# Kernel tuning notes

Measured on AMD Instinct MI355X. Metric: run time of the kernel, lower is better.

Reference implementation:

```python
import jax, jax.numpy as jnp
import numpy as np

EPS = float(np.finfo(np.float32).eps)


def setup_inputs() -> dict:
    key = jax.random.key(0)
    k1, k2, k3, k4 = jax.random.split(key, 4)
    B, M, N = 16, 200000, 200000
    xyzs1 = jax.random.normal(k1, (B, M, 3), dtype=jnp.float32)
    xyzs2 = jax.random.normal(k2, (B, M, 3), dtype=jnp.float32)
    pred_pairs = jax.random.randint(k3, (B, N, 2), 0, M)
    weights = jax.random.uniform(k4, (B, 1, N), dtype=jnp.float32)
    return {"xyzs1": xyzs1, "xyzs2": xyzs2, "pred_pairs": pred_pairs, "weights": weights}


def _weighted_procrustes(X, Y, w):
    # X, Y: [B, N, 3]; w: [B, N, 1]. DGR-style weighted Kabsch/Procrustes.
    W1 = jnp.abs(w).sum(axis=1, keepdims=True)            # [B, 1, 1]
    w_norm = w / (W1 + EPS)                               # [B, N, 1]
    mux = (w_norm * X).sum(axis=1, keepdims=True)         # [B, 1, 3]
    muy = (w_norm * Y).sum(axis=1, keepdims=True)         # [B, 1, 3]
    # Sxy = (Y - muy)^T @ (w_norm * (X - mux)) per sample -> [B, 3, 3]
    Sxy = jnp.einsum('bni,bnj->bij', Y - muy, w_norm * (X - mux))
    U, _, Vh = jnp.linalg.svd(Sxy)                        # Sxy = U diag(s) Vh
    # reflection fix: diag(1, 1, sign(det(U) * det(V)))
    d = jnp.where(jnp.linalg.det(U) * jnp.linalg.det(Vh) < 0, -1.0, 1.0)  # [B]
    S = jnp.concatenate([jnp.ones((X.shape[0], 2), dtype=U.dtype), d[:, None]], axis=1)
    R = (U * S[:, None, :]) @ Vh                          # U @ diag(S) @ V^T
    t = muy[:, 0, :] - jnp.einsum('bij,bj->bi', R, mux[:, 0, :])  # [B, 3]
    return R, t


def reference(xyzs1, xyzs2, pred_pairs, weights):
    w = jnp.transpose(weights, (0, 2, 1))                 # [B, N, 1]
    # batched gather of correspondences
    X = jax.vmap(lambda pts, idx: pts[idx])(xyzs1, pred_pairs[:, :, 0])
    Y = jax.vmap(lambda pts, idx: pts[idx])(xyzs2, pred_pairs[:, :, 1])
    Rs, ts = _weighted_procrustes(X, Y, w)
    ws = w.sum(axis=(1, 2))                               # per-sample weight sums
    return Rs, ts, ws
```

## Files before the change

### kernel.cpp

```cpp
#include <hip/hip_runtime.h>
#include <math.h>

#define BPB 96
#define NACC 17

typedef float  floatx4 __attribute__((ext_vector_type(4)));
typedef unsigned long long ullx2 __attribute__((ext_vector_type(2)));

struct __attribute__((packed, aligned(4))) f4 { float x, y, z, w; };

__device__ __forceinline__ void gather_pt(const float* __restrict__ base, int idx,
                                          bool guard, int M1,
                                          float& p0, float& p1, float& p2)
{
    const size_t o = 3 * (size_t)idx;
    if (guard && __builtin_expect(idx == M1, 0)) {
        p0 = base[o]; p1 = base[o + 1]; p2 = base[o + 2];
    } else {
        const f4 v = *(const f4*)(base + o);
        p0 = v.x; p1 = v.y; p2 = v.z;
    }
}

template <bool GUARD>
__device__ __forceinline__ void wp_loop(
    const float* __restrict__ x1b, const float* __restrict__ x2b,
    const ullx2* __restrict__ pv, const floatx4* __restrict__ wv,
    int c0, int stride, int nChunks, int M1, float acc[NACC])
{
    for (int c = c0; c < nChunks; c += stride) {
        const ullx2  pA = __builtin_nontemporal_load(&pv[2 * c]);
        const ullx2  pB = __builtin_nontemporal_load(&pv[2 * c + 1]);
        const floatx4 w4 = __builtin_nontemporal_load(&wv[c]);

        int ix[4], iy[4];
        ix[0] = (int)(unsigned)(pA.x & 0xffffffffu); iy[0] = (int)(unsigned)(pA.x >> 32);
        ix[1] = (int)(unsigned)(pA.y & 0xffffffffu); iy[1] = (int)(unsigned)(pA.y >> 32);
        ix[2] = (int)(unsigned)(pB.x & 0xffffffffu); iy[2] = (int)(unsigned)(pB.x >> 32);
        ix[3] = (int)(unsigned)(pB.y & 0xffffffffu); iy[3] = (int)(unsigned)(pB.y >> 32);

        float X[4][3], Y[4][3];
#pragma unroll
        for (int u = 0; u < 4; ++u)
            gather_pt(x1b, ix[u], GUARD, M1, X[u][0], X[u][1], X[u][2]);
#pragma unroll
        for (int u = 0; u < 4; ++u)
            gather_pt(x2b, iy[u], GUARD, M1, Y[u][0], Y[u][1], Y[u][2]);

#pragma unroll
        for (int u = 0; u < 4; ++u) {
            const float w = w4[u];
            acc[0] += fabsf(w);
            acc[1] += w;
            acc[2] += w * X[u][0];
            acc[3] += w * X[u][1];
            acc[4] += w * X[u][2];
            const float wy0 = w * Y[u][0], wy1 = w * Y[u][1], wy2 = w * Y[u][2];
            acc[5] += wy0; acc[6] += wy1; acc[7] += wy2;
            acc[8]  += wy0 * X[u][0]; acc[9]  += wy0 * X[u][1]; acc[10] += wy0 * X[u][2];
            acc[11] += wy1 * X[u][0]; acc[12] += wy1 * X[u][1]; acc[13] += wy1 * X[u][2];
            acc[14] += wy2 * X[u][0]; acc[15] += wy2 * X[u][1]; acc[16] += wy2 * X[u][2];
        }
    }
}

__global__ __launch_bounds__(256) void wp_partials(
    const float* __restrict__ xyzs1,
    const float* __restrict__ xyzs2,
    const int*   __restrict__ pairs,
    const float* __restrict__ weights,
    float* __restrict__ partials,
    int B, int M, int N)
{
    int b, ib;
    if ((B & 7) == 0) {
        const int grp = blockIdx.x / (8 * BPB);
        const int r   = blockIdx.x % (8 * BPB);
        b  = grp * 8 + (r & 7);
        ib = r >> 3;
    } else {
        b  = blockIdx.x % B;
        ib = blockIdx.x / B;
    }
    const int tid = threadIdx.x;

    const float* __restrict__ x1b = xyzs1 + (size_t)b * M * 3;
    const float* __restrict__ x2b = xyzs2 + (size_t)b * M * 3;
    const ullx2* __restrict__ pv  = (const ullx2*)(pairs + (size_t)b * N * 2);
    const floatx4* __restrict__ wv = (const floatx4*)(weights + (size_t)b * N);

    const bool lastBatch = (b == B - 1);
    const int  M1 = M - 1;
    const int  nChunks = N >> 2;

    float acc[NACC];
#pragma unroll
    for (int k = 0; k < NACC; ++k) acc[k] = 0.f;

    const int c0 = ib * 256 + tid;
    if (lastBatch)
        wp_loop<true >(x1b, x2b, pv, wv, c0, BPB * 256, nChunks, M1, acc);
    else
        wp_loop<false>(x1b, x2b, pv, wv, c0, BPB * 256, nChunks, M1, acc);

    const int* pb = (const int*)pv;
    const float* wb = (const float*)wv;
    for (int n = (nChunks << 2) + ib * 256 + tid; n < N; n += BPB * 256) {
        const int ixt = pb[2 * n], iyt = pb[2 * n + 1];
        const float w = wb[n];
        float X0, X1, X2, Y0, Y1, Y2;
        gather_pt(x1b, ixt, true, M1, X0, X1, X2);
        gather_pt(x2b, iyt, true, M1, Y0, Y1, Y2);
        acc[0] += fabsf(w); acc[1] += w;
        acc[2] += w * X0; acc[3] += w * X1; acc[4] += w * X2;
        const float wy0 = w * Y0, wy1 = w * Y1, wy2 = w * Y2;
        acc[5] += wy0; acc[6] += wy1; acc[7] += wy2;
        acc[8]  += wy0 * X0; acc[9]  += wy0 * X1; acc[10] += wy0 * X2;
        acc[11] += wy1 * X0; acc[12] += wy1 * X1; acc[13] += wy1 * X2;
        acc[14] += wy2 * X0; acc[15] += wy2 * X1; acc[16] += wy2 * X2;
    }

#pragma unroll
    for (int k = 0; k < NACC; ++k) {
#pragma unroll
        for (int off = 32; off > 0; off >>= 1)
            acc[k] += __shfl_down(acc[k], off);
    }

    __shared__ float red[4][NACC];
    const int wave = tid >> 6, lane = tid & 63;
    if (lane == 0) {
#pragma unroll
        for (int k = 0; k < NACC; ++k) red[wave][k] = acc[k];
    }
    __syncthreads();
    if (tid < NACC) {
        const float s = red[0][tid] + red[1][tid] + red[2][tid] + red[3][tid];
        partials[((size_t)b * BPB + ib) * NACC + tid] = s;
    }
}

__global__ __launch_bounds__(64) void wp_finalize(
    const float* __restrict__ partials,
    float* __restrict__ out,
    int B)
{
    const int b = blockIdx.x;
    const int t = threadIdx.x;

    double acc[NACC];
#pragma unroll
    for (int k = 0; k < NACC; ++k) acc[k] = 0.0;

    const float* __restrict__ p = partials + (size_t)b * BPB * NACC;
    for (int i = t; i < BPB; i += 64) {
#pragma unroll
        for (int k = 0; k < NACC; ++k) acc[k] += (double)p[i * NACC + k];
    }
#pragma unroll
    for (int k = 0; k < NACC; ++k) {
#pragma unroll
        for (int off = 32; off > 0; off >>= 1)
            acc[k] += __shfl_down(acc[k], off);
    }

    if (t != 0) return;

    const double EPS = 1.1920928955078125e-07;
    const double W1 = acc[0];
    const double Sw = acc[1];
    const double inv = 1.0 / (W1 + EPS);
    const double mux[3] = {acc[2] * inv, acc[3] * inv, acc[4] * inv};
    const double muy[3] = {acc[5] * inv, acc[6] * inv, acc[7] * inv};
    const double S0 = Sw * inv;
    const double c2 = 2.0 - S0;

    double S[3][3];
#pragma unroll
    for (int i = 0; i < 3; ++i)
#pragma unroll
        for (int j = 0; j < 3; ++j)
            S[i][j] = acc[8 + i * 3 + j] * inv - muy[i] * mux[j] * c2;

    double A[3][3];
#pragma unroll
    for (int i = 0; i < 3; ++i)
#pragma unroll
        for (int j = 0; j < 3; ++j)
            A[i][j] = S[0][i] * S[0][j] + S[1][i] * S[1][j] + S[2][i] * S[2][j];

    double V[3][3] = {{1, 0, 0}, {0, 1, 0}, {0, 0, 1}};
    for (int sweep = 0; sweep < 30; ++sweep) {
        const double offd = fabs(A[0][1]) + fabs(A[0][2]) + fabs(A[1][2]);
        if (offd == 0.0) break;
        for (int pq = 0; pq < 3; ++pq) {
            const int pi = (pq == 2) ? 1 : 0;
            const int qi = (pq == 0) ? 1 : 2;
            const double apq = A[pi][qi];
            if (fabs(apq) < 1e-300) continue;
            const double theta = (A[qi][qi] - A[pi][pi]) / (2.0 * apq);
            const double tt = copysign(1.0, theta) / (fabs(theta) + sqrt(theta * theta + 1.0));
            const double c = 1.0 / sqrt(tt * tt + 1.0);
            const double s = tt * c;
            const int r = 3 - pi - qi;
            A[pi][pi] -= tt * apq;
            A[qi][qi] += tt * apq;
            A[pi][qi] = A[qi][pi] = 0.0;
            const double arp = A[r][pi], arq = A[r][qi];
            A[r][pi] = A[pi][r] = c * arp - s * arq;
            A[r][qi] = A[qi][r] = s * arp + c * arq;
#pragma unroll
            for (int k = 0; k < 3; ++k) {
                const double vkp = V[k][pi], vkq = V[k][qi];
                V[k][pi] = c * vkp - s * vkq;
                V[k][qi] = s * vkp + c * vkq;
            }
        }
    }

    double lam[3] = {A[0][0], A[1][1], A[2][2]};
    int idx[3] = {0, 1, 2};
    if (lam[idx[0]] < lam[idx[1]]) { int q = idx[0]; idx[0] = idx[1]; idx[1] = q; }
    if (lam[idx[0]] < lam[idx[2]]) { int q = idx[0]; idx[0] = idx[2]; idx[2] = q; }
    if (lam[idx[1]] < lam[idx[2]]) { int q = idx[1]; idx[1] = idx[2]; idx[2] = q; }

    const double v0[3] = {V[0][idx[0]], V[1][idx[0]], V[2][idx[0]]};
    const double v1[3] = {V[0][idx[1]], V[1][idx[1]], V[2][idx[1]]};

    double u0[3], u1[3];
#pragma unroll
    for (int i = 0; i < 3; ++i) u0[i] = S[i][0] * v0[0] + S[i][1] * v0[1] + S[i][2] * v0[2];
    {
        const double n2 = u0[0] * u0[0] + u0[1] * u0[1] + u0[2] * u0[2];
        const double in0 = 1.0 / sqrt(fmax(n2, 1e-300));
        u0[0] *= in0; u0[1] *= in0; u0[2] *= in0;
    }
#pragma unroll
    for (int i = 0; i < 3; ++i) u1[i] = S[i][0] * v1[0] + S[i][1] * v1[1] + S[i][2] * v1[2];
    {
        const double d01 = u1[0] * u0[0] + u1[1] * u0[1] + u1[2] * u0[2];
        u1[0] -= d01 * u0[0]; u1[1] -= d01 * u0[1]; u1[2] -= d01 * u0[2];
        const double n2 = u1[0] * u1[0] + u1[1] * u1[1] + u1[2] * u1[2];
        const double in1 = 1.0 / sqrt(fmax(n2, 1e-300));
        u1[0] *= in1; u1[1] *= in1; u1[2] *= in1;
    }
    const double u2[3] = {u0[1] * u1[2] - u0[2] * u1[1],
                          u0[2] * u1[0] - u0[0] * u1[2],
                          u0[0] * u1[1] - u0[1] * u1[0]};
    const double v2[3] = {v0[1] * v1[2] - v0[2] * v1[1],
                          v0[2] * v1[0] - v0[0] * v1[2],
                          v0[0] * v1[1] - v0[1] * v1[0]};

    double R[3][3];
#pragma unroll
    for (int i = 0; i < 3; ++i)
#pragma unroll
        for (int j = 0; j < 3; ++j)
            R[i][j] = u0[i] * v0[j] + u1[i] * v1[j] + u2[i] * v2[j];

    double tv[3];
#pragma unroll
    for (int i = 0; i < 3; ++i)
        tv[i] = muy[i] - (R[i][0] * mux[0] + R[i][1] * mux[1] + R[i][2] * mux[2]);

    float* __restrict__ Rout = out + (size_t)b * 9;
#pragma unroll
    for (int i = 0; i < 3; ++i)
#pragma unroll
        for (int j = 0; j < 3; ++j)
            Rout[i * 3 + j] = (float)R[i][j];
    float* __restrict__ tout = out + (size_t)B * 9 + (size_t)b * 3;
#pragma unroll
    for (int i = 0; i < 3; ++i) tout[i] = (float)tv[i];
    out[(size_t)B * 12 + b] = (float)Sw;
}

extern "C" void kernel_launch(void* const* d_in, const int* in_sizes, int n_in,
                              void* d_out, int out_size, void* d_ws, size_t ws_size,
                              hipStream_t stream) {
    const float* xyzs1   = (const float*)d_in[0];
    const float* xyzs2   = (const float*)d_in[1];
    const int*   pairs   = (const int*)d_in[2];
    const float* weights = (const float*)d_in[3];
    float* out = (float*)d_out;

    const int B = out_size / 13;
    const int M = in_sizes[0] / (3 * B);
    const int N = in_sizes[3] / B;

    float* partials = (float*)d_ws;

    hipLaunchKernelGGL(wp_partials, dim3(B * BPB), dim3(256), 0, stream,
                       xyzs1, xyzs2, pairs, weights, partials, B, M, N);
    hipLaunchKernelGGL(wp_finalize, dim3(B), dim3(64), 0, stream,
                       partials, out, B);
}
```

Measured before the change: 72.53 us.

## Split gather-reduce into two passes, one per point set, via workspace records

Splits the single kernel into a pass that gathers only from the first point cloud and writes weighted coordinates and second-cloud indices to workspace, and a second pass that gathers from the second cloud and accumulates the cross-covariance. The aim is to halve each pass's random-gather working set for better cache hit rates. It adds a large intermediate write and read, plus an extra launch, and raises blocks per batch. The old path is kept as a fallback when workspace is too small.

```diff
diff --git a/kernel.cpp b/kernel.cpp
--- a/kernel.cpp
+++ b/kernel.cpp
@@ -1,10 +1,11 @@
 #include <hip/hip_runtime.h>
 #include <math.h>
 
-#define BPB 96
+#define BPB 128
 #define NACC 17
 
 typedef float  floatx4 __attribute__((ext_vector_type(4)));
+typedef int    intx4   __attribute__((ext_vector_type(4)));
 typedef unsigned long long ullx2 __attribute__((ext_vector_type(2)));
 
 struct __attribute__((packed, aligned(4))) f4 { float x, y, z, w; };
@@ -22,57 +23,8 @@
     }
 }
 
-template <bool GUARD>
-__device__ __forceinline__ void wp_loop(
-    const float* __restrict__ x1b, const float* __restrict__ x2b,
-    const ullx2* __restrict__ pv, const floatx4* __restrict__ wv,
-    int c0, int stride, int nChunks, int M1, float acc[NACC])
-{
-    for (int c = c0; c < nChunks; c += stride) {
-        const ullx2  pA = __builtin_nontemporal_load(&pv[2 * c]);
-        const ullx2  pB = __builtin_nontemporal_load(&pv[2 * c + 1]);
-        const floatx4 w4 = __builtin_nontemporal_load(&wv[c]);
-
-        int ix[4], iy[4];
-        ix[0] = (int)(unsigned)(pA.x & 0xffffffffu); iy[0] = (int)(unsigned)(pA.x >> 32);
-        ix[1] = (int)(unsigned)(pA.y & 0xffffffffu); iy[1] = (int)(unsigned)(pA.y >> 32);
-        ix[2] = (int)(unsigned)(pB.x & 0xffffffffu); iy[2] = (int)(unsigned)(pB.x >> 32);
-        ix[3] = (int)(unsigned)(pB.y & 0xffffffffu); iy[3] = (int)(unsigned)(pB.y >> 32);
-
-        float X[4][3], Y[4][3];
-#pragma unroll
-        for (int u = 0; u < 4; ++u)
-            gather_pt(x1b, ix[u], GUARD, M1, X[u][0], X[u][1], X[u][2]);
-#pragma unroll
-        for (int u = 0; u < 4; ++u)
-            gather_pt(x2b, iy[u], GUARD, M1, Y[u][0], Y[u][1], Y[u][2]);
-
-#pragma unroll
-        for (int u = 0; u < 4; ++u) {
-            const float w = w4[u];
-            acc[0] += fabsf(w);
-            acc[1] += w;
-            acc[2] += w * X[u][0];
-            acc[3] += w * X[u][1];
-            acc[4] += w * X[u][2];
-            const float wy0 = w * Y[u][0], wy1 = w * Y[u][1], wy2 = w * Y[u][2];
-            acc[5] += wy0; acc[6] += wy1; acc[7] += wy2;
-            acc[8]  += wy0 * X[u][0]; acc[9]  += wy0 * X[u][1]; acc[10] += wy0 * X[u][2];
-            acc[11] += wy1 * X[u][0]; acc[12] += wy1 * X[u][1]; acc[13] += wy1 * X[u][2];
-            acc[14] += wy2 * X[u][0]; acc[15] += wy2 * X[u][1]; acc[16] += wy2 * X[u][2];
-        }
-    }
-}
-
-__global__ __launch_bounds__(256) void wp_partials(
-    const float* __restrict__ xyzs1,
-    const float* __restrict__ xyzs2,
-    const int*   __restrict__ pairs,
-    const float* __restrict__ weights,
-    float* __restrict__ partials,
-    int B, int M, int N)
-{
-    int b, ib;
+__device__ __forceinline__ void xcd_map(int B, int& b, int& ib)
+{
     if ((B & 7) == 0) {
         const int grp = blockIdx.x / (8 * BPB);
         const int r   = blockIdx.x % (8 * BPB);
@@ -82,27 +34,261 @@
         b  = blockIdx.x % B;
         ib = blockIdx.x / B;
     }
+}
+
+template <bool GUARD>
+__device__ __forceinline__ void p1_loop(
+    const float* __restrict__ x1b,
+    const ullx2* __restrict__ pv, const floatx4* __restrict__ wv,
+    floatx4* __restrict__ recb, intx4* __restrict__ jvb,
+    int c0, int stride, int nChunks, int M1, float acc[5])
+{
+    for (int c = c0; c < nChunks; c += stride) {
+        const ullx2  pA = __builtin_nontemporal_load(&pv[2 * c]);
+        const ullx2  pB = __builtin_nontemporal_load(&pv[2 * c + 1]);
+        const floatx4 w4 = __builtin_nontemporal_load(&wv[c]);
+
+        int ix[4];
+        intx4 j4;
+        ix[0] = (int)(unsigned)(pA.x & 0xffffffffu); j4.x = (int)(unsigned)(pA.x >> 32);
+        ix[1] = (int)(unsigned)(pA.y & 0xffffffffu); j4.y = (int)(unsigned)(pA.y >> 32);
+        ix[2] = (int)(unsigned)(pB.x & 0xffffffffu); j4.z = (int)(unsigned)(pB.x >> 32);
+        ix[3] = (int)(unsigned)(pB.y & 0xffffffffu); j4.w = (int)(unsigned)(pB.y >> 32);
+
+        float X[4][3];
+#pragma unroll
+        for (int u = 0; u < 4; ++u)
+            gather_pt(x1b, ix[u], GUARD, M1, X[u][0], X[u][1], X[u][2]);
+
+#pragma unroll
+        for (int u = 0; u < 4; ++u) {
+            const float w = w4[u];
+            acc[0] += fabsf(w);
+            acc[1] += w;
+            const float wx0 = w * X[u][0], wx1 = w * X[u][1], wx2 = w * X[u][2];
+            acc[2] += wx0; acc[3] += wx1; acc[4] += wx2;
+            floatx4 r; r.x = wx0; r.y = wx1; r.z = wx2; r.w = w;
+            __builtin_nontemporal_store(r, &recb[4 * c + u]);
+        }
+        __builtin_nontemporal_store(j4, &jvb[c]);
+    }
+}
+
+__global__ __launch_bounds__(256) void wp_pass1(
+    const float* __restrict__ xyzs1,
+    const int*   __restrict__ pairs,
+    const float* __restrict__ weights,
+    floatx4* __restrict__ recs,
+    intx4*   __restrict__ jarr,
+    float* __restrict__ partials,
+    int B, int M, int N)
+{
+    int b, ib; xcd_map(B, b, ib);
     const int tid = threadIdx.x;
 
+    const float* __restrict__ x1b = xyzs1 + (size_t)b * M * 3;
+    const ullx2* __restrict__ pv  = (const ullx2*)(pairs + (size_t)b * N * 2);
+    const floatx4* __restrict__ wv = (const floatx4*)(weights + (size_t)b * N);
+    floatx4* __restrict__ recb = recs + (size_t)b * N;
+    intx4*   __restrict__ jvb  = jarr + ((size_t)b * N >> 2);
+
+    const bool lastBatch = (b == B - 1);
+    const int  M1 = M - 1;
+    const int  nChunks = N >> 2;
+
+    float acc[5];
+#pragma unroll
+    for (int k = 0; k < 5; ++k) acc[k] = 0.f;
+
+    const int c0 = ib * 256 + tid;
+    if (lastBatch) p1_loop<true >(x1b, pv, wv, recb, jvb, c0, BPB * 256, nChunks, M1, acc);
+    else           p1_loop<false>(x1b, pv, wv, recb, jvb, c0, BPB * 256, nChunks, M1, acc);
+
+    const int* pb = (const int*)pv;
+    const float* wb = (const float*)wv;
+    float* recf = (float*)recb;
+    int*   jf   = (int*)jvb;
+    for (int n = (nChunks << 2) + ib * 256 + tid; n < N; n += BPB * 256) {
+        const int ixt = pb[2 * n], iyt = pb[2 * n + 1];
+        const float w = wb[n];
+        float X0, X1, X2;
+        gather_pt(x1b, ixt, true, M1, X0, X1, X2);
+        acc[0] += fabsf(w); acc[1] += w;
+        const float wx0 = w * X0, wx1 = w * X1, wx2 = w * X2;
+        acc[2] += wx0; acc[3] += wx1; acc[4] += wx2;
+        recf[4 * n] = wx0; recf[4 * n + 1] = wx1; recf[4 * n + 2] = wx2; recf[4 * n + 3] = w;
+        jf[n] = iyt;
+    }
+
+#pragma unroll
+    for (int k = 0; k < 5; ++k) {
+#pragma unroll
+        for (int off = 32; off > 0; off >>= 1)
+            acc[k] += __shfl_down(acc[k], off);
+    }
+    __shared__ float red[4][5];
+    const int wave = tid >> 6, lane = tid & 63;
+    if (lane == 0) {
+#pragma unroll
+        for (int k = 0; k < 5; ++k) red[wave][k] = acc[k];
+    }
+    __syncthreads();
+    if (tid < 5) {
+        const float s = red[0][tid] + red[1][tid] + red[2][tid] + red[3][tid];
+        partials[((size_t)b * BPB + ib) * NACC + tid] = s;
+    }
+}
+
+template <bool GUARD>
+__device__ __forceinline__ void p2_loop(
+    const float* __restrict__ x2b,
+    const floatx4* __restrict__ recb, const intx4* __restrict__ jvb,
+    int c0, int stride, int nChunks, int M1, float acc[12])
+{
+    for (int c = c0; c < nChunks; c += stride) {
+        const intx4 j4 = __builtin_nontemporal_load(&jvb[c]);
+        floatx4 r[4];
+#pragma unroll
+        for (int u = 0; u < 4; ++u)
+            r[u] = __builtin_nontemporal_load(&recb[4 * c + u]);
+
+        int jy[4] = {j4.x, j4.y, j4.z, j4.w};
+        float Y[4][3];
+#pragma unroll
+        for (int u = 0; u < 4; ++u)
+            gather_pt(x2b, jy[u], GUARD, M1, Y[u][0], Y[u][1], Y[u][2]);
+
+#pragma unroll
+        for (int u = 0; u < 4; ++u) {
+            const float w = r[u].w;
+            acc[0] += w * Y[u][0];
+            acc[1] += w * Y[u][1];
+            acc[2] += w * Y[u][2];
+#pragma unroll
+            for (int i = 0; i < 3; ++i) {
+                acc[3 + 3 * i]     += Y[u][i] * r[u].x;
+                acc[3 + 3 * i + 1] += Y[u][i] * r[u].y;
+                acc[3 + 3 * i + 2] += Y[u][i] * r[u].z;
+            }
+        }
+    }
+}
+
+__global__ __launch_bounds__(256) void wp_pass2(
+    const float* __restrict__ xyzs2,
+    const floatx4* __restrict__ recs,
+    const intx4*   __restrict__ jarr,
+    float* __restrict__ partials,
+    int B, int M, int N)
+{
+    int b, ib; xcd_map(B, b, ib);
+    const int tid = threadIdx.x;
+
+    const float* __restrict__ x2b = xyzs2 + (size_t)b * M * 3;
+    const floatx4* __restrict__ recb = recs + (size_t)b * N;
+    const intx4*   __restrict__ jvb  = jarr + ((size_t)b * N >> 2);
+
+    const bool lastBatch = (b == B - 1);
+    const int  M1 = M - 1;
+    const int  nChunks = N >> 2;
+
+    float acc[12];
+#pragma unroll
+    for (int k = 0; k < 12; ++k) acc[k] = 0.f;
+
+    const int c0 = ib * 256 + tid;
+    if (lastBatch) p2_loop<true >(x2b, recb, jvb, c0, BPB * 256, nChunks, M1, acc);
+    else           p2_loop<false>(x2b, recb, jvb, c0, BPB * 256, nChunks, M1, acc);
+
+    const float* recf = (const float*)recb;
+    const int*   jf   = (const int*)jvb;
+    for (int n = (nChunks << 2) + ib * 256 + tid; n < N; n += BPB * 256) {
+        const int jyt = jf[n];
+        const float wx0 = recf[4 * n], wx1 = recf[4 * n + 1], wx2 = recf[4 * n + 2], w = recf[4 * n + 3];
+        float Y0, Y1, Y2;
+        gather_pt(x2b, jyt, true, M1, Y0, Y1, Y2);
+        acc[0] += w * Y0; acc[1] += w * Y1; acc[2] += w * Y2;
+        acc[3] += Y0 * wx0; acc[4]  += Y0 * wx1; acc[5]  += Y0 * wx2;
+        acc[6] += Y1 * wx0; acc[7]  += Y1 * wx1; acc[8]  += Y1 * wx2;
+        acc[9] += Y2 * wx0; acc[10] += Y2 * wx1; acc[11] += Y2 * wx2;
+    }
+
+#pragma unroll
+    for (int k = 0; k < 12; ++k) {
+#pragma unroll
+        for (int off = 32; off > 0; off >>= 1)
+            acc[k] += __shfl_down(acc[k], off);
+    }
+    __shared__ float red[4][12];
+    const int wave = tid >> 6, lane = tid & 63;
+    if (lane == 0) {
+#pragma unroll
+        for (int k = 0; k < 12; ++k) red[wave][k] = acc[k];
+    }
+    __syncthreads();
+    if (tid < 12) {
+        const float s = red[0][tid] + red[1][tid] + red[2][tid] + red[3][tid];
+        partials[((size_t)b * BPB + ib) * NACC + 5 + tid] = s;
+    }
+}
+
+template <bool GUARD>
+__device__ __forceinline__ void wp_loop1(
+    const float* __restrict__ x1b, const float* __restrict__ x2b,
+    const ullx2* __restrict__ pv, const floatx4* __restrict__ wv,
+    int c0, int stride, int nChunks, int M1, float acc[NACC])
+{
+    for (int c = c0; c < nChunks; c += stride) {
+        const ullx2  pA = __builtin_nontemporal_load(&pv[2 * c]);
+        const ullx2  pB = __builtin_nontemporal_load(&pv[2 * c + 1]);
+        const floatx4 w4 = __builtin_nontemporal_load(&wv[c]);
+        int ix[4], iy[4];
+        ix[0] = (int)(unsigned)(pA.x & 0xffffffffu); iy[0] = (int)(unsigned)(pA.x >> 32);
+        ix[1] = (int)(unsigned)(pA.y & 0xffffffffu); iy[1] = (int)(unsigned)(pA.y >> 32);
+        ix[2] = (int)(unsigned)(pB.x & 0xffffffffu); iy[2] = (int)(unsigned)(pB.x >> 32);
+        ix[3] = (int)(unsigned)(pB.y & 0xffffffffu); iy[3] = (int)(unsigned)(pB.y >> 32);
+        float X[4][3], Y[4][3];
+#pragma unroll
+        for (int u = 0; u < 4; ++u) gather_pt(x1b, ix[u], GUARD, M1, X[u][0], X[u][1], X[u][2]);
+#pragma unroll
+        for (int u = 0; u < 4; ++u) gather_pt(x2b, iy[u], GUARD, M1, Y[u][0], Y[u][1], Y[u][2]);
+#pragma unroll
+        for (int u = 0; u < 4; ++u) {
+            const float w = w4[u];
+            acc[0] += fabsf(w); acc[1] += w;
+            acc[2] += w * X[u][0]; acc[3] += w * X[u][1]; acc[4] += w * X[u][2];
+            const float wy0 = w * Y[u][0], wy1 = w * Y[u][1], wy2 = w * Y[u][2];
+            acc[5] += wy0; acc[6] += wy1; acc[7] += wy2;
+            acc[8]  += wy0 * X[u][0]; acc[9]  += wy0 * X[u][1]; acc[10] += wy0 * X[u][2];
+            acc[11] += wy1 * X[u][0]; acc[12] += wy1 * X[u][1]; acc[13] += wy1 * X[u][2];
+            acc[14] += wy2 * X[u][0]; acc[15] += wy2 * X[u][1]; acc[16] += wy2 * X[u][2];
+        }
+    }
+}
+
+__global__ __launch_bounds__(256) void wp_partials(
+    const float* __restrict__ xyzs1,
+    const float* __restrict__ xyzs2,
+    const int*   __restrict__ pairs,
+    const float* __restrict__ weights,
+    float* __restrict__ partials,
+    int B, int M, int N)
+{
+    int b, ib; xcd_map(B, b, ib);
+    const int tid = threadIdx.x;
     const float* __restrict__ x1b = xyzs1 + (size_t)b * M * 3;
     const float* __restrict__ x2b = xyzs2 + (size_t)b * M * 3;
     const ullx2* __restrict__ pv  = (const ullx2*)(pairs + (size_t)b * N * 2);
     const floatx4* __restrict__ wv = (const floatx4*)(weights + (size_t)b * N);
-
     const bool lastBatch = (b == B - 1);
     const int  M1 = M - 1;
     const int  nChunks = N >> 2;
-
     float acc[NACC];
 #pragma unroll
     for (int k = 0; k < NACC; ++k) acc[k] = 0.f;
-
     const int c0 = ib * 256 + tid;
-    if (lastBatch)
-        wp_loop<true >(x1b, x2b, pv, wv, c0, BPB * 256, nChunks, M1, acc);
-    else
-        wp_loop<false>(x1b, x2b, pv, wv, c0, BPB * 256, nChunks, M1, acc);
-
+    if (lastBatch) wp_loop1<true >(x1b, x2b, pv, wv, c0, BPB * 256, nChunks, M1, acc);
+    else           wp_loop1<false>(x1b, x2b, pv, wv, c0, BPB * 256, nChunks, M1, acc);
     const int* pb = (const int*)pv;
     const float* wb = (const float*)wv;
     for (int n = (nChunks << 2) + ib * 256 + tid; n < N; n += BPB * 256) {
@@ -119,14 +305,12 @@
         acc[11] += wy1 * X0; acc[12] += wy1 * X1; acc[13] += wy1 * X2;
         acc[14] += wy2 * X0; acc[15] += wy2 * X1; acc[16] += wy2 * X2;
     }
-
 #pragma unroll
     for (int k = 0; k < NACC; ++k) {
 #pragma unroll
         for (int off = 32; off > 0; off >>= 1)
             acc[k] += __shfl_down(acc[k], off);
     }
-
     __shared__ float red[4][NACC];
     const int wave = tid >> 6, lane = tid & 63;
     if (lane == 0) {
@@ -288,10 +472,25 @@
     const int M = in_sizes[0] / (3 * B);
     const int N = in_sizes[3] / B;
 
-    float* partials = (float*)d_ws;
-
-    hipLaunchKernelGGL(wp_partials, dim3(B * BPB), dim3(256), 0, stream,
-                       xyzs1, xyzs2, pairs, weights, partials, B, M, N);
-    hipLaunchKernelGGL(wp_finalize, dim3(B), dim3(64), 0, stream,
-                       partials, out, B);
-}
+    const size_t recBytes  = (size_t)B * N * 16;
+    const size_t jBytes    = (size_t)B * N * 4;
+    const size_t partBytes = (size_t)B * BPB * NACC * 4;
+
+    if (ws_size >= recBytes + jBytes + partBytes) {
+        floatx4* recs = (floatx4*)d_ws;
+        intx4*   jarr = (intx4*)((char*)d_ws + recBytes);
+        float* partials = (float*)((char*)d_ws + recBytes + jBytes);
+        hipLaunchKernelGGL(wp_pass1, dim3(B * BPB), dim3(256), 0, stream,
+                           xyzs1, pairs, weights, recs, jarr, partials, B, M, N);
+        hipLaunchKernelGGL(wp_pass2, dim3(B * BPB), dim3(256), 0, stream,
+                           xyzs2, recs, jarr, partials, B, M, N);
+        hipLaunchKernelGGL(wp_finalize, dim3(B), dim3(64), 0, stream,
+                           partials, out, B);
+    } else {
+        float* partials = (float*)d_ws;
+        hipLaunchKernelGGL(wp_partials, dim3(B * BPB), dim3(256), 0, stream,
+                           xyzs1, xyzs2, pairs, weights, partials, B, M, N);
+        hipLaunchKernelGGL(wp_finalize, dim3(B), dim3(64), 0, stream,
+                           partials, out, B);
+    }
+}
```

Result: slower. 119.1 us (+64.3%).

## Unroll gather loop by three chunks with branchless boundary handling and fewer blocks

Applied to the files above, without the earlier changes.

Restructures the main accumulation loop to issue index, weight and point loads for three chunks per iteration, so each thread keeps more gathers in flight. The last-point guard becomes branchless: the 16-byte load is shifted back by one float when the index is M-1 and the components are selected, which removes the templated two-path loop. Blocks per batch drop from 96 to 64 and launch bounds request two blocks per CU. The cost is higher register pressure from 24 live f4 gathers plus 17 accumulators, which could spill or lower occupancy.

```diff
diff --git a/kernel.cpp b/kernel.cpp
--- a/kernel.cpp
+++ b/kernel.cpp
@@ -1,70 +1,30 @@
 #include <hip/hip_runtime.h>
 #include <math.h>
 
-#define BPB 96
+#define BPB  64
 #define NACC 17
+#define UNR  3
 
 typedef float  floatx4 __attribute__((ext_vector_type(4)));
 typedef unsigned long long ullx2 __attribute__((ext_vector_type(2)));
 
 struct __attribute__((packed, aligned(4))) f4 { float x, y, z, w; };
 
-__device__ __forceinline__ void gather_pt(const float* __restrict__ base, int idx,
-                                          bool guard, int M1,
-                                          float& p0, float& p1, float& p2)
+__device__ __forceinline__ void acc_pair(float acc[NACC], float w,
+                                         float X0, float X1, float X2,
+                                         float Y0, float Y1, float Y2)
 {
-    const size_t o = 3 * (size_t)idx;
-    if (guard && __builtin_expect(idx == M1, 0)) {
-        p0 = base[o]; p1 = base[o + 1]; p2 = base[o + 2];
-    } else {
-        const f4 v = *(const f4*)(base + o);
-        p0 = v.x; p1 = v.y; p2 = v.z;
-    }
+    acc[0] += fabsf(w);
+    acc[1] += w;
+    acc[2] += w * X0; acc[3] += w * X1; acc[4] += w * X2;
+    const float wy0 = w * Y0, wy1 = w * Y1, wy2 = w * Y2;
+    acc[5] += wy0; acc[6] += wy1; acc[7] += wy2;
+    acc[8]  += wy0 * X0; acc[9]  += wy0 * X1; acc[10] += wy0 * X2;
+    acc[11] += wy1 * X0; acc[12] += wy1 * X1; acc[13] += wy1 * X2;
+    acc[14] += wy2 * X0; acc[15] += wy2 * X1; acc[16] += wy2 * X2;
 }
 
-template <bool GUARD>
-__device__ __forceinline__ void wp_loop(
-    const float* __restrict__ x1b, const float* __restrict__ x2b,
-    const ullx2* __restrict__ pv, const floatx4* __restrict__ wv,
-    int c0, int stride, int nChunks, int M1, float acc[NACC])
-{
-    for (int c = c0; c < nChunks; c += stride) {
-        const ullx2  pA = __builtin_nontemporal_load(&pv[2 * c]);
-        const ullx2  pB = __builtin_nontemporal_load(&pv[2 * c + 1]);
-        const floatx4 w4 = __builtin_nontemporal_load(&wv[c]);
-
-        int ix[4], iy[4];
-        ix[0] = (int)(unsigned)(pA.x & 0xffffffffu); iy[0] = (int)(unsigned)(pA.x >> 32);
-        ix[1] = (int)(unsigned)(pA.y & 0xffffffffu); iy[1] = (int)(unsigned)(pA.y >> 32);
-        ix[2] = (int)(unsigned)(pB.x & 0xffffffffu); iy[2] = (int)(unsigned)(pB.x >> 32);
-        ix[3] = (int)(unsigned)(pB.y & 0xffffffffu); iy[3] = (int)(unsigned)(pB.y >> 32);
-
-        float X[4][3], Y[4][3];
-#pragma unroll
-        for (int u = 0; u < 4; ++u)
-            gather_pt(x1b, ix[u], GUARD, M1, X[u][0], X[u][1], X[u][2]);
-#pragma unroll
-        for (int u = 0; u < 4; ++u)
-            gather_pt(x2b, iy[u], GUARD, M1, Y[u][0], Y[u][1], Y[u][2]);
-
-#pragma unroll
-        for (int u = 0; u < 4; ++u) {
-            const float w = w4[u];
-            acc[0] += fabsf(w);
-            acc[1] += w;
-            acc[2] += w * X[u][0];
-            acc[3] += w * X[u][1];
-            acc[4] += w * X[u][2];
-            const float wy0 = w * Y[u][0], wy1 = w * Y[u][1], wy2 = w * Y[u][2];
-            acc[5] += wy0; acc[6] += wy1; acc[7] += wy2;
-            acc[8]  += wy0 * X[u][0]; acc[9]  += wy0 * X[u][1]; acc[10] += wy0 * X[u][2];
-            acc[11] += wy1 * X[u][0]; acc[12] += wy1 * X[u][1]; acc[13] += wy1 * X[u][2];
-            acc[14] += wy2 * X[u][0]; acc[15] += wy2 * X[u][1]; acc[16] += wy2 * X[u][2];
-        }
-    }
-}
-
-__global__ __launch_bounds__(256) void wp_partials(
+__global__ __launch_bounds__(256, 2) void wp_partials(
     const float* __restrict__ xyzs1,
     const float* __restrict__ xyzs2,
     const int*   __restrict__ pairs,
@@ -89,35 +49,109 @@
     const ullx2* __restrict__ pv  = (const ullx2*)(pairs + (size_t)b * N * 2);
     const floatx4* __restrict__ wv = (const floatx4*)(weights + (size_t)b * N);
 
-    const bool lastBatch = (b == B - 1);
-    const int  M1 = M - 1;
-    const int  nChunks = N >> 2;
+    const int M1 = M - 1;
+    const int nChunks = N >> 2;
+    const int S = BPB * 256;
 
     float acc[NACC];
 #pragma unroll
     for (int k = 0; k < NACC; ++k) acc[k] = 0.f;
 
-    const int c0 = ib * 256 + tid;
-    if (lastBatch)
-        wp_loop<true >(x1b, x2b, pv, wv, c0, BPB * 256, nChunks, M1, acc);
-    else
-        wp_loop<false>(x1b, x2b, pv, wv, c0, BPB * 256, nChunks, M1, acc);
+    int c = ib * 256 + tid;
+
+    for (; c + (UNR - 1) * S < nChunks; c += UNR * S) {
+        ullx2 pA[UNR], pB[UNR];
+        floatx4 w4[UNR];
+#pragma unroll
+        for (int u = 0; u < UNR; ++u) {
+            const int cu = c + u * S;
+            pA[u] = __builtin_nontemporal_load(&pv[2 * cu]);
+            pB[u] = __builtin_nontemporal_load(&pv[2 * cu + 1]);
+            w4[u] = __builtin_nontemporal_load(&wv[cu]);
+        }
+
+        int ix[4 * UNR], iy[4 * UNR];
+#pragma unroll
+        for (int u = 0; u < UNR; ++u) {
+            ix[4 * u]     = (int)(unsigned)(pA[u].x & 0xffffffffu);
+            iy[4 * u]     = (int)(unsigned)(pA[u].x >> 32);
+            ix[4 * u + 1] = (int)(unsigned)(pA[u].y & 0xffffffffu);
+            iy[4 * u + 1] = (int)(unsigned)(pA[u].y >> 32);
+            ix[4 * u + 2] = (int)(unsigned)(pB[u].x & 0xffffffffu);
+            iy[4 * u + 2] = (int)(unsigned)(pB[u].x >> 32);
+            ix[4 * u + 3] = (int)(unsigned)(pB[u].y & 0xffffffffu);
+            iy[4 * u + 3] = (int)(unsigned)(pB[u].y >> 32);
+        }
+
+        f4 VX[4 * UNR], VY[4 * UNR];
+        int lx[4 * UNR], ly[4 * UNR];
+#pragma unroll
+        for (int k = 0; k < 4 * UNR; ++k) {
+            lx[k] = (ix[k] == M1) ? 1 : 0;
+            VX[k] = *(const f4*)(x1b + (3 * (size_t)ix[k] - lx[k]));
+        }
+#pragma unroll
+        for (int k = 0; k < 4 * UNR; ++k) {
+            ly[k] = (iy[k] == M1) ? 1 : 0;
+            VY[k] = *(const f4*)(x2b + (3 * (size_t)iy[k] - ly[k]));
+        }
+
+#pragma unroll
+        for (int k = 0; k < 4 * UNR; ++k) {
+            const float X0 = lx[k] ? VX[k].y : VX[k].x;
+            const float X1 = lx[k] ? VX[k].z : VX[k].y;
+            const float X2 = lx[k] ? VX[k].w : VX[k].z;
+            const float Y0 = ly[k] ? VY[k].y : VY[k].x;
+            const float Y1 = ly[k] ? VY[k].z : VY[k].y;
+            const float Y2 = ly[k] ? VY[k].w : VY[k].z;
+            acc_pair(acc, w4[k >> 2][k & 3], X0, X1, X2, Y0, Y1, Y2);
+        }
+    }
+
+    for (; c < nChunks; c += S) {
+        const ullx2 pA = __builtin_nontemporal_load(&pv[2 * c]);
+        const ullx2 pB = __builtin_nontemporal_load(&pv[2 * c + 1]);
+        const floatx4 w4 = __builtin_nontemporal_load(&wv[c]);
+        int ix[4], iy[4];
+        ix[0] = (int)(unsigned)(pA.x & 0xffffffffu); iy[0] = (int)(unsigned)(pA.x >> 32);
+        ix[1] = (int)(unsigned)(pA.y & 0xffffffffu); iy[1] = (int)(unsigned)(pA.y >> 32);
+        ix[2] = (int)(unsigned)(pB.x & 0xffffffffu); iy[2] = (int)(unsigned)(pB.x >> 32);
+        ix[3] = (int)(unsigned)(pB.y & 0xffffffffu); iy[3] = (int)(unsigned)(pB.y >> 32);
+        f4 VX[4], VY[4];
+        int lx[4], ly[4];
+#pragma unroll
+        for (int k = 0; k < 4; ++k) {
+            lx[k] = (ix[k] == M1) ? 1 : 0;
+            VX[k] = *(const f4*)(x1b + (3 * (size_t)ix[k] - lx[k]));
+        }
+#pragma unroll
+        for (int k = 0; k < 4; ++k) {
+            ly[k] = (iy[k] == M1) ? 1 : 0;
+            VY[k] = *(const f4*)(x2b + (3 * (size_t)iy[k] - ly[k]));
+        }
+#pragma unroll
+        for (int k = 0; k < 4; ++k) {
+            const float X0 = lx[k] ? VX[k].y : VX[k].x;
+            const float X1 = lx[k] ? VX[k].z : VX[k].y;
+            const float X2 = lx[k] ? VX[k].w : VX[k].z;
+            const float Y0 = ly[k] ? VY[k].y : VY[k].x;
+            const float Y1 = ly[k] ? VY[k].z : VY[k].y;
+            const float Y2 = ly[k] ? VY[k].w : VY[k].z;
+            acc_pair(acc, w4[k], X0, X1, X2, Y0, Y1, Y2);
+        }
+    }
 
     const int* pb = (const int*)pv;
     const float* wb = (const float*)wv;
-    for (int n = (nChunks << 2) + ib * 256 + tid; n < N; n += BPB * 256) {
-        const int ixt = pb[2 * n], iyt = pb[2 * n + 1];
+    for (int n = (nChunks << 2) + ib * 256 + tid; n < N; n += S) {
+        const int i0 = pb[2 * n], j0 = pb[2 * n + 1];
         const float w = wb[n];
-        float X0, X1, X2, Y0, Y1, Y2;
-        gather_pt(x1b, ixt, true, M1, X0, X1, X2);
-        gather_pt(x2b, iyt, true, M1, Y0, Y1, Y2);
-        acc[0] += fabsf(w); acc[1] += w;
-        acc[2] += w * X0; acc[3] += w * X1; acc[4] += w * X2;
-        const float wy0 = w * Y0, wy1 = w * Y1, wy2 = w * Y2;
-        acc[5] += wy0; acc[6] += wy1; acc[7] += wy2;
-        acc[8]  += wy0 * X0; acc[9]  += wy0 * X1; acc[10] += wy0 * X2;
-        acc[11] += wy1 * X0; acc[12] += wy1 * X1; acc[13] += wy1 * X2;
-        acc[14] += wy2 * X0; acc[15] += wy2 * X1; acc[16] += wy2 * X2;
+        const int li = (i0 == M1) ? 1 : 0, lj = (j0 == M1) ? 1 : 0;
+        const f4 vx = *(const f4*)(x1b + (3 * (size_t)i0 - li));
+        const f4 vy = *(const f4*)(x2b + (3 * (size_t)j0 - lj));
+        acc_pair(acc, w,
+                 li ? vx.y : vx.x, li ? vx.z : vx.y, li ? vx.w : vx.z,
+                 lj ? vy.y : vy.x, lj ? vy.z : vy.y, lj ? vy.w : vy.z);
     }
 
 #pragma unroll
@@ -200,20 +234,20 @@
             if (fabs(apq) < 1e-300) continue;
             const double theta = (A[qi][qi] - A[pi][pi]) / (2.0 * apq);
             const double tt = copysign(1.0, theta) / (fabs(theta) + sqrt(theta * theta + 1.0));
-            const double c = 1.0 / sqrt(tt * tt + 1.0);
-            const double s = tt * c;
+            const double cc = 1.0 / sqrt(tt * tt + 1.0);
+            const double ss = tt * cc;
             const int r = 3 - pi - qi;
             A[pi][pi] -= tt * apq;
             A[qi][qi] += tt * apq;
             A[pi][qi] = A[qi][pi] = 0.0;
             const double arp = A[r][pi], arq = A[r][qi];
-            A[r][pi] = A[pi][r] = c * arp - s * arq;
-            A[r][qi] = A[qi][r] = s * arp + c * arq;
+            A[r][pi] = A[pi][r] = cc * arp - ss * arq;
+            A[r][qi] = A[qi][r] = ss * arp + cc * arq;
 #pragma unroll
             for (int k = 0; k < 3; ++k) {
                 const double vkp = V[k][pi], vkq = V[k][qi];
-                V[k][pi] = c * vkp - s * vkq;
-                V[k][qi] = s * vkp + c * vkq;
+                V[k][pi] = cc * vkp - ss * vkq;
+                V[k][qi] = ss * vkp + cc * vkq;
             }
         }
     }
```

After: 70.80 us. 2.4% less time.
